# Kernel tuning notes

Measured on AMD Instinct MI355X. Metric: run time of the kernel, lower is better.

Reference implementation:

```python
import jax, jax.numpy as jnp
import numpy as np

N = 100000   # nodes
E = 1000000  # edges
G = 64       # graphs in batch
DIN, DH, DOUT = 128, 128, 64
BN_EPS = 1e-5


def setup_inputs() -> dict:
    key = jax.random.key(0)
    ks = jax.random.split(key, 20)
    inp = {}
    inp['x'] = jax.random.normal(ks[0], (N, DIN), dtype=jnp.float32)
    inp['edge_index'] = jax.random.randint(ks[1], (2, E), 0, N, dtype=jnp.int64)
    inp['batch'] = jnp.sort(jax.random.randint(ks[2], (N,), 0, G, dtype=jnp.int64))
    # GCN conv weights (stored [in, out]) + biases
    s = lambda k, i, o: jax.random.normal(k, (i, o), dtype=jnp.float32) / np.sqrt(i)
    inp['W1'] = s(ks[3], DIN, DH);  inp['b1'] = jnp.zeros((DH,), jnp.float32)
    inp['W2'] = s(ks[4], DH, DH);   inp['b2'] = jnp.zeros((DH,), jnp.float32)
    inp['W3'] = s(ks[5], DH, DOUT); inp['b3'] = jnp.zeros((DOUT,), jnp.float32)
    # BatchNorm params/buffers (eval mode)
    inp['g1'] = jnp.ones((DH,), jnp.float32);  inp['beta1'] = jnp.zeros((DH,), jnp.float32)
    inp['g2'] = jnp.ones((DH,), jnp.float32);  inp['beta2'] = jnp.zeros((DH,), jnp.float32)
    inp['mean1'] = jnp.zeros((DH,), jnp.float32); inp['var1'] = jnp.ones((DH,), jnp.float32)
    inp['mean2'] = jnp.zeros((DH,), jnp.float32); inp['var2'] = jnp.ones((DH,), jnp.float32)
    # GlobalAttention gate_nn: Linear(DOUT,DH) ReLU Linear(DH,1)
    inp['Wg1'] = s(ks[6], DOUT, DH); inp['bg1'] = jnp.zeros((DH,), jnp.float32)
    inp['Wg2'] = s(ks[7], DH, 1);    inp['bg2'] = jnp.zeros((1,), jnp.float32)
    # head MLP: Linear(DOUT,DH) ReLU Linear(DH,DOUT)
    inp['Wm1'] = s(ks[8], DOUT, DH); inp['bm1'] = jnp.zeros((DH,), jnp.float32)
    inp['Wm2'] = s(ks[9], DH, DOUT); inp['bm2'] = jnp.zeros((DOUT,), jnp.float32)
    return inp


def _gcn_conv(x, W, b, src, dst):
    # PyG GCNConv: add self-loops, sym-normalize, linear, scatter-sum, bias
    h = x @ W                                            # [N, out]
    deg = jnp.ones((N,), h.dtype).at[dst].add(1.0)       # in-degree + self-loop
    dinv = jax.lax.rsqrt(deg)
    norm = dinv[src] * dinv[dst]                         # [E]
    msg = h[src] * norm[:, None]                         # gather + scale
    out = jax.ops.segment_sum(msg, dst, num_segments=N)  # scatter
    out = out + h * (dinv * dinv)[:, None]               # self-loop term
    return out + b


def _bn(x, g, beta, mean, var):
    return (x - mean) * jax.lax.rsqrt(var + BN_EPS) * g + beta


def reference(x, edge_index, batch, W1, b1, W2, b2, W3, b3,
              g1, beta1, g2, beta2, mean1, var1, mean2, var2,
              Wg1, bg1, Wg2, bg2, Wm1, bm1, Wm2, bm2):
    src, dst = edge_index[0], edge_index[1]
    h = jax.nn.relu(_bn(_gcn_conv(x, W1, b1, src, dst), g1, beta1, mean1, var1))
    h = jax.nn.relu(_bn(_gcn_conv(h, W2, b2, src, dst), g2, beta2, mean2, var2))
    h = _gcn_conv(h, W3, b3, src, dst)                   # [N, DOUT]
    # GlobalAttention pooling: per-graph softmax of gate scores
    gate = jax.nn.relu(h @ Wg1 + bg1) @ Wg2 + bg2        # [N, 1]
    gate = gate[:, 0]
    m = jax.ops.segment_max(gate, batch, num_segments=G)
    e = jnp.exp(gate - m[batch])
    s = jax.ops.segment_sum(e, batch, num_segments=G)
    a = e / s[batch]                                     # [N]
    pooled = jax.ops.segment_sum(h * a[:, None], batch, num_segments=G)  # [G, DOUT]
    # MLP head (dropout off in eval)
    return jax.nn.relu(pooled @ Wm1 + bm1) @ Wm2 + bm2   # [G, DOUT]
```

## Files before the change

kernel.cpp:

```cpp
#include <hip/hip_runtime.h>
#include <hip/hip_bf16.h>
#include <hip/hip_fp16.h>
#include <math.h>

#define NN 100000
#define EE 1000000
#define GG 64
#define BN_EPS 1e-5f
#define CPB 16
#define EB 4096
#define NBLK ((EE + EB - 1) / EB)
#define NBUCK ((NN + 511) / 512)

typedef __attribute__((ext_vector_type(8))) short bf16x8;
typedef __attribute__((ext_vector_type(4))) float f32x4;

__device__ inline short f2bf(float f) {
  unsigned u = __float_as_uint(f);
  u = u + 0x7fff + ((u >> 16) & 1);
  return (short)(u >> 16);
}
__device__ inline float bf2f(short h) {
  return __uint_as_float(((unsigned)(unsigned short)h) << 16);
}

__device__ inline unsigned fenc(float f) {
  int b = __float_as_int(f);
  return (b < 0) ? ~(unsigned)b : ((unsigned)b | 0x80000000u);
}
__device__ inline float fdec(unsigned u) {
  int b = (u & 0x80000000u) ? (int)(u & 0x7fffffffu) : (int)~u;
  return __int_as_float(b);
}

__device__ inline void acc2(float& a0, float& a1, unsigned u) {
  asm("v_fma_mix_f32 %0, %2, 1.0, %0 op_sel:[0,0,0] op_sel_hi:[1,0,0]\n\t"
      "v_fma_mix_f32 %1, %2, 1.0, %1 op_sel:[1,0,0] op_sel_hi:[1,0,0]"
      : "+v"(a0), "+v"(a1)
      : "v"(u));
}
__device__ inline void acc8(float* a, uint4 u) {
  acc2(a[0], a[1], u.x);
  acc2(a[2], a[3], u.y);
  acc2(a[4], a[5], u.z);
  acc2(a[6], a[7], u.w);
}
__device__ inline uint4 zsel(uint4 u, int ok) {
  uint4 r;
  r.x = ok ? u.x : 0u;
  r.y = ok ? u.y : 0u;
  r.z = ok ? u.z : 0u;
  r.w = ok ? u.w : 0u;
  return r;
}

__global__ __launch_bounds__(256) void k_bhist(const int* __restrict__ dst,
                                               int* __restrict__ bhist, int E) {
  __shared__ int h[256];
  int t = threadIdx.x;
  h[t] = 0;
  __syncthreads();
  int base = blockIdx.x * EB;
#pragma unroll
  for (int j = 0; j < EB / 256; ++j) {
    int i = base + j * 256 + t;
    if (i < E) atomicAdd(&h[dst[i] >> 9], 1);
  }
  __syncthreads();
  bhist[blockIdx.x * 256 + t] = h[t];
}

__global__ __launch_bounds__(256) void k_bscan1(int* __restrict__ bhist,
                                                int* __restrict__ btot) {
  __shared__ int s[256];
  int bin = blockIdx.x, t = threadIdx.x;
  int v = (t < NBLK) ? bhist[t * 256 + bin] : 0;
  s[t] = v;
  __syncthreads();
  for (int o = 1; o < 256; o <<= 1) {
    int u = (t >= o) ? s[t - o] : 0;
    __syncthreads();
    s[t] += u;
    __syncthreads();
  }
  if (t < NBLK) bhist[t * 256 + bin] = s[t] - v;
  if (t == 255) btot[bin] = s[255];
}

__global__ __launch_bounds__(256) void k_bscan2(const int* __restrict__ btot,
                                                int* __restrict__ bstart) {
  __shared__ int s[256];
  int t = threadIdx.x;
  int v = btot[t];
  s[t] = v;
  __syncthreads();
  for (int o = 1; o < 256; o <<= 1) {
    int u = (t >= o) ? s[t - o] : 0;
    __syncthreads();
    s[t] += u;
    __syncthreads();
  }
  bstart[t] = s[t] - v;
}

__global__ __launch_bounds__(256) void k_bscat(const int* __restrict__ src,
                                               const int* __restrict__ dst,
                                               const int* __restrict__ bhist,
                                               const int* __restrict__ bstart,
                                               int2* __restrict__ pairs, int E) {
  __shared__ int h[256];
  __shared__ int base[256];
  int t = threadIdx.x;
  h[t] = 0;
  __syncthreads();
  int b0 = blockIdx.x * EB;
  int ds[EB / 256], rk[EB / 256];
#pragma unroll
  for (int j = 0; j < EB / 256; ++j) {
    int i = b0 + j * 256 + t;
    if (i < E) {
      int d = dst[i];
      ds[j] = d;
      rk[j] = atomicAdd(&h[d >> 9], 1);
    } else
      ds[j] = -1;
  }
  __syncthreads();
  base[t] = bstart[t] + bhist[blockIdx.x * 256 + t];
  __syncthreads();
#pragma unroll
  for (int j = 0; j < EB / 256; ++j) {
    int i = b0 + j * 256 + t;
    if (ds[j] >= 0) {
      int pos = base[ds[j] >> 9] + rk[j];
      pairs[pos] = make_int2(src[i], ds[j]);
    }
  }
}

__global__ __launch_bounds__(256) void k_bfill(const int2* __restrict__ pairs,
                                               const int* __restrict__ bstart,
                                               int* __restrict__ rowstart,
                                               int* __restrict__ eidx,
                                               float* __restrict__ dinv, int N,
                                               int E) {
  __shared__ int h[512];
  __shared__ int ex[512];
  __shared__ int ps[256];
  const int b = blockIdx.x;
  const int n0 = b << 9;
  const int e0 = bstart[b], e1 = bstart[b + 1];
  const int t = threadIdx.x;
  h[t] = 0;
  h[t + 256] = 0;
  __syncthreads();
  for (int i = e0 + t; i < e1; i += 256) atomicAdd(&h[pairs[i].y - n0], 1);
  __syncthreads();
  int v0 = h[2 * t], v1 = h[2 * t + 1];
  int sp = v0 + v1;
  ps[t] = sp;
  __syncthreads();
  for (int o = 1; o < 256; o <<= 1) {
    int u = (t >= o) ? ps[t - o] : 0;
    __syncthreads();
    ps[t] += u;
    __syncthreads();
  }
  int ex0 = ps[t] - sp;
  ex[2 * t] = ex0;
  ex[2 * t + 1] = ex0 + v0;
  __syncthreads();
  for (int i = t; i < 512; i += 256) {
    int node = n0 + i;
    if (node < N) {
      rowstart[node] = e0 + ex[i];
      dinv[node] = rsqrtf(1.0f + (float)h[i]);
    }
  }
  if (b == 0 && t == 0) rowstart[N] = E;
  __syncthreads();
  for (int i = e0 + t; i < e1; i += 256) {
    int2 p = pairs[i];
    int r = atomicAdd(&ex[p.y - n0], 1);
    eidx[e0 + r] = p.x;
  }
}

__global__ __launch_bounds__(256) void k_prep(
    const float* __restrict__ W1, const float* __restrict__ W2,
    const float* __restrict__ W3, const float* __restrict__ Wg1,
    short* __restrict__ wt, const float* __restrict__ g1,
    const float* __restrict__ b1, const float* __restrict__ m1,
    const float* __restrict__ v1, const float* __restrict__ g2,
    const float* __restrict__ b2, const float* __restrict__ m2,
    const float* __restrict__ v2, float* __restrict__ s1,
    float* __restrict__ h1, float* __restrict__ s2, float* __restrict__ h2,
    const int* __restrict__ batch, int* __restrict__ gstart,
    float* __restrict__ pooledw, int N) {
  const int b = blockIdx.x, t = threadIdx.x;
  if (b < 192) {
    int i = b * 256 + t;
    const float* W;
    short *hi, *lo;
    int K, M, idx;
    if (i < 16384) {
      W = W1; hi = wt; lo = wt + 16384; K = 128; M = 128; idx = i;
    } else if (i < 32768) {
      W = W2; hi = wt + 32768; lo = wt + 49152; K = 128; M = 128; idx = i - 16384;
    } else if (i < 40960) {
      W = W3; hi = wt + 65536; lo = wt + 73728; K = 128; M = 64; idx = i - 32768;
    } else {
      W = Wg1; hi = wt + 81920; lo = wt + 90112; K = 64; M = 128; idx = i - 40960;
    }
    int k = idx / M, n = idx % M;
    float w = W[idx];
    short h = f2bf(w);
    hi[n * K + k] = h;
    lo[n * K + k] = f2bf(w - bf2f(h));
  } else if (b == 192) {
    if (t < 128) {
      float s = g1[t] * rsqrtf(v1[t] + BN_EPS);
      s1[t] = s;
      h1[t] = b1[t] - m1[t] * s;
    } else {
      int j = t - 128;
      float s = g2[j] * rsqrtf(v2[j] + BN_EPS);
      s2[j] = s;
      h2[j] = b2[j] - m2[j] * s;
    }
  } else {
    if (t <= GG) {
      int lo = 0, hi = N;
      while (lo < hi) {
        int mid = (lo + hi) >> 1;
        if (batch[mid] < t) lo = mid + 1;
        else hi = mid;
      }
      gstart[t] = lo;
    }
    for (int i = t; i < GG * 64 + GG + GG; i += 256) pooledw[i] = 0.f;
  }
}

template <int K, int M, int CTB, int AIN, int DINV, int GATE, int OUTH>
__device__ __forceinline__ void mgemm_body(
    short* lds, const float* __restrict__ Xf, const short* __restrict__ Xhi,
    const short* __restrict__ Xlo, const short* __restrict__ Wthi,
    const short* __restrict__ Wtlo, const float* __restrict__ dinv,
    const float* __restrict__ gbias, const float* __restrict__ Wg2v,
    const float* __restrict__ bg2v, void* __restrict__ Y,
    float* __restrict__ gate, int nrows) {
  constexpr int NC = K / 32;
  constexpr int KP = K + 8;
  constexpr int R = 2;
  const int lane = threadIdx.x & 63;
  const int wave = threadIdx.x >> 6;
  const int m16 = lane & 15;
  const int quad = lane >> 4;
  const int rowbase = blockIdx.x * 128 + wave * 32;
  const int cbase = blockIdx.y * CTB * 16;

  bf16x8 ahi[R][NC], alo[R][NC];
#pragma unroll
  for (int t = 0; t < R; ++t) {
    const int arow = rowbase + t * 16 + m16;
    const bool rok = arow < nrows;
#pragma unroll
    for (int c = 0; c < NC; ++c) {
      const int k0 = c * 32 + quad * 8;
      if constexpr (AIN) {
        if (rok) {
          ahi[t][c] = *(const bf16x8*)(Xhi + (size_t)arow * K + k0);
          alo[t][c] = *(const bf16x8*)(Xlo + (size_t)arow * K + k0);
        } else {
          ahi[t][c] = bf16x8{0, 0, 0, 0, 0, 0, 0, 0};
          alo[t][c] = bf16x8{0, 0, 0, 0, 0, 0, 0, 0};
        }
      } else {
        float4 v0 = make_float4(0.f, 0.f, 0.f, 0.f), v1 = v0;
        if (rok) {
          v0 = *(const float4*)(Xf + (size_t)arow * K + k0);
          v1 = *(const float4*)(Xf + (size_t)arow * K + k0 + 4);
        }
        float vv[8] = {v0.x, v0.y, v0.z, v0.w, v1.x, v1.y, v1.z, v1.w};
#pragma unroll
        for (int j = 0; j < 8; ++j) {
          short h = f2bf(vv[j]);
          ahi[t][c][j] = h;
          alo[t][c][j] = f2bf(vv[j] - bf2f(h));
        }
      }
    }
  }

  {
    constexpr int ELEMS = CTB * 16 * K;
#pragma unroll
    for (int i = threadIdx.x * 8; i < ELEMS; i += 256 * 8) {
      const int r = i / K, c = i % K;
      *(bf16x8*)(&lds[r * KP + c]) =
          *(const bf16x8*)(Wthi + (size_t)(cbase + r) * K + c);
      *(bf16x8*)(&lds[CTB * 16 * KP + r * KP + c]) =
          *(const bf16x8*)(Wtlo + (size_t)(cbase + r) * K + c);
    }
  }

  float dv[R][4];
  if constexpr (DINV && !GATE) {
#pragma unroll
    for (int t = 0; t < R; ++t)
#pragma unroll
      for (int r = 0; r < 4; ++r) {
        int row = rowbase + t * 16 + quad * 4 + r;
        dv[t][r] = (row < nrows) ? dinv[row] : 0.f;
      }
  }

  float gp[R][4];
  if constexpr (GATE) {
#pragma unroll
    for (int t = 0; t < R; ++t)
#pragma unroll
      for (int r = 0; r < 4; ++r) gp[t][r] = 0.f;
  }

  __syncthreads();

  f32x4 accs[CTB][R];
#pragma unroll
  for (int ct = 0; ct < CTB; ++ct) {
    bf16x8 bhi[NC], blo[NC];
    const int wrow = (ct * 16 + m16) * KP + quad * 8;
#pragma unroll
    for (int c = 0; c < NC; ++c) {
      bhi[c] = *(const bf16x8*)(&lds[wrow + c * 32]);
      blo[c] = *(const bf16x8*)(&lds[CTB * 16 * KP + wrow + c * 32]);
    }
#pragma unroll
    for (int t = 0; t < R; ++t) {
      f32x4 acc = {0.f, 0.f, 0.f, 0.f};
#pragma unroll
      for (int c = 0; c < NC; ++c) {
        acc = __builtin_amdgcn_mfma_f32_16x16x32_bf16(ahi[t][c], bhi[c], acc, 0, 0, 0);
        acc = __builtin_amdgcn_mfma_f32_16x16x32_bf16(ahi[t][c], blo[c], acc, 0, 0, 0);
        acc = __builtin_amdgcn_mfma_f32_16x16x32_bf16(alo[t][c], bhi[c], acc, 0, 0, 0);
      }
      if constexpr (GATE) {
        const int col = cbase + ct * 16 + m16;
        const float gb = gbias[col], wg = Wg2v[col];
#pragma unroll
        for (int r = 0; r < 4; ++r) gp[t][r] += fmaxf(acc[r] + gb, 0.f) * wg;
      } else {
        accs[ct][t] = acc;
      }
    }
  }

  if constexpr (GATE) {
#pragma unroll
    for (int o = 1; o < 16; o <<= 1) {
#pragma unroll
      for (int t = 0; t < R; ++t)
#pragma unroll
        for (int r = 0; r < 4; ++r) gp[t][r] += __shfl_xor(gp[t][r], o, 64);
    }
    if (m16 == 0) {
      const float b2 = bg2v[0];
#pragma unroll
      for (int t = 0; t < R; ++t)
#pragma unroll
        for (int r = 0; r < 4; ++r) {
          const int row = rowbase + t * 16 + quad * 4 + r;
          if (row < nrows) gate[row] = gp[t][r] + b2;
        }
    }
  } else {
    constexpr int COLS = CTB * 16;
    constexpr int SP = COLS + 8;
    __syncthreads();
#pragma unroll
    for (int ct = 0; ct < CTB; ++ct)
#pragma unroll
      for (int t = 0; t < R; ++t)
#pragma unroll
        for (int r = 0; r < 4; ++r) {
          const int row_l = wave * 32 + t * 16 + quad * 4 + r;
          float v = accs[ct][t][r];
          if constexpr (DINV) v *= dv[t][r];
          __half hv = __float2half(v);
          lds[row_l * SP + ct * 16 + m16] = *(short*)&hv;
        }
    __syncthreads();
    constexpr int TOT = 128 * COLS;
#pragma unroll
    for (int p = 0; p < TOT / (256 * 8); ++p) {
      const int idx8 = (p * 256 + threadIdx.x) * 8;
      const int row_l = idx8 / COLS;
      const int col0 = idx8 % COLS;
      const int grow = blockIdx.x * 128 + row_l;
      if (grow < nrows) {
        bf16x8 v = *(const bf16x8*)(&lds[row_l * SP + col0]);
        *(bf16x8*)((__half*)Y + (size_t)grow * M + cbase + col0) = v;
      }
    }
  }
}

#define MGEMM_ARGS                                                            \
  const float *Xf, const short *Xhi, const short *Xlo, const short *Wthi,     \
      const short *Wtlo, const float *dinv, const float *gbias,               \
      const float *Wg2v, const float *bg2v, void *Y, float *gate, int nrows

#define DEF_MGEMM(NAME, K, M, CTB, AIN, DINV, GATE, OUTH, WPE)                \
  __global__ __launch_bounds__(256, WPE) void NAME(MGEMM_ARGS) {              \
    __shared__ short lds[2 * CTB * 16 * (K + 8)];                             \
    mgemm_body<K, M, CTB, AIN, DINV, GATE, OUTH>(lds, Xf, Xhi, Xlo, Wthi,     \
                                                 Wtlo, dinv, gbias, Wg2v,     \
                                                 bg2v, Y, gate, nrows);       \
  }

DEF_MGEMM(k_mgemm1, 128, 128, 2, 0, 1, 0, 1, 4)
DEF_MGEMM(k_mgemm2, 128, 128, 2, 1, 1, 0, 1, 4)
DEF_MGEMM(k_mgemm3, 128, 64, 2, 1, 1, 0, 1, 4)
DEF_MGEMM(k_mgemmg, 64, 128, 8, 0, 0, 1, 0, 3)

template <int M, int EPI>
__device__ __forceinline__ void agg_body(
    const __half* __restrict__ hp, const int* __restrict__ rowstart,
    const int* __restrict__ eidx, const float* __restrict__ dinv,
    const float* __restrict__ bias, const float* __restrict__ bns,
    const float* __restrict__ bnh, float* __restrict__ outf,
    short* __restrict__ ohi, short* __restrict__ olo, int N) {
  constexpr int LPR = M / 8;
  constexpr int NPW = 64 / (2 * LPR);
  const int wv = (blockIdx.x * 256 + threadIdx.x) >> 6;
  const int lane = threadIdx.x & 63;
  const int grp = lane / (2 * LPR);
  const int slot = (lane / LPR) & 1;
  const int sub = lane % LPR;
  const int w = wv * NPW + grp;
  if (w >= N) return;
  const unsigned subo = (unsigned)sub * 16u;
  const float di = dinv[w];
  const int lo = rowstart[w], hi = rowstart[w + 1];
  const int hi1 = hi - 1;
  const char* hpb = (const char*)hp;
  float a[8] = {0.f, 0.f, 0.f, 0.f, 0.f, 0.f, 0.f, 0.f};

  int e = lo + slot;
  while (e < hi) {
    int idx[8], ss[8];
    uint4 uu[8];
#pragma unroll
    for (int p = 0; p < 8; ++p) {
      idx[p] = e + 2 * p;
      ss[p] = eidx[min(idx[p], hi1)];
    }
#pragma unroll
    for (int p = 0; p < 8; ++p)
      uu[p] = *(const uint4*)(hpb + ((unsigned)ss[p] * (unsigned)(M * 2) + subo));
#pragma unroll
    for (int p = 0; p < 8; ++p) {
      uu[p] = zsel(uu[p], idx[p] < hi);
      acc8(a, uu[p]);
    }
    e += 16;
  }
#pragma unroll
  for (int j = 0; j < 8; ++j) a[j] += __shfl_xor(a[j], LPR, 64);

  if (slot != 0) return;
  uint4 us = *(const uint4*)(hpb + ((unsigned)w * (unsigned)(M * 2) + subo));
  acc8(a, us);
  float4 b0 = *(const float4*)(bias + sub * 8);
  float4 b1 = *(const float4*)(bias + sub * 8 + 4);
  float r[8];
  r[0] = a[0] * di + b0.x;
  r[1] = a[1] * di + b0.y;
  r[2] = a[2] * di + b0.z;
  r[3] = a[3] * di + b0.w;
  r[4] = a[4] * di + b1.x;
  r[5] = a[5] * di + b1.y;
  r[6] = a[6] * di + b1.z;
  r[7] = a[7] * di + b1.w;
  if constexpr (EPI) {
    float4 s0 = *(const float4*)(bns + sub * 8);
    float4 s1 = *(const float4*)(bns + sub * 8 + 4);
    float4 h0 = *(const float4*)(bnh + sub * 8);
    float4 h1 = *(const float4*)(bnh + sub * 8 + 4);
    float sv[8] = {s0.x, s0.y, s0.z, s0.w, s1.x, s1.y, s1.z, s1.w};
    float hv[8] = {h0.x, h0.y, h0.z, h0.w, h1.x, h1.y, h1.z, h1.w};
    short hs[8], ls[8];
#pragma unroll
    for (int j = 0; j < 8; ++j) {
      float ev = fmaxf(r[j] * sv[j] + hv[j], 0.f);
      short hb = f2bf(ev);
      float res = ev - bf2f(hb);
      hs[j] = hb;
      ls[j] = (short)(__float_as_uint(res) >> 16);
    }
    *(short4*)(ohi + (size_t)w * M + sub * 8) = make_short4(hs[0], hs[1], hs[2], hs[3]);
    *(short4*)(ohi + (size_t)w * M + sub * 8 + 4) = make_short4(hs[4], hs[5], hs[6], hs[7]);
    *(short4*)(olo + (size_t)w * M + sub * 8) = make_short4(ls[0], ls[1], ls[2], ls[3]);
    *(short4*)(olo + (size_t)w * M + sub * 8 + 4) = make_short4(ls[4], ls[5], ls[6], ls[7]);
  } else {
    *(float4*)(outf + (size_t)w * M + sub * 8) = make_float4(r[0], r[1], r[2], r[3]);
    *(float4*)(outf + (size_t)w * M + sub * 8 + 4) = make_float4(r[4], r[5], r[6], r[7]);
  }
}

#define AGG_ARGS                                                              \
  const __half *hp, const int *rowstart, const int *eidx, const float *dinv,  \
      const float *bias, const float *bns, const float *bnh, float *outf,     \
      short *ohi, short *olo, int N

#define DEF_AGG(NAME, M, EPI)                                                 \
  __global__ __launch_bounds__(256) void NAME(AGG_ARGS) {                     \
    agg_body<M, EPI>(hp, rowstart, eidx, dinv, bias, bns, bnh, outf, ohi,     \
                     olo, N);                                                 \
  }

DEF_AGG(k_agg1, 128, 1)
DEF_AGG(k_agg2, 128, 1)
DEF_AGG(k_agg3, 64, 0)

__global__ __launch_bounds__(256) void k_pmax(const float* __restrict__ gate,
                                              const int* __restrict__ gstart,
                                              unsigned* __restrict__ gmaxu) {
  __shared__ unsigned red[256];
  const int g = blockIdx.x / CPB;
  const int c = blockIdx.x % CPB;
  const int lo = gstart[g], hi = gstart[g + 1];
  const int len = hi - lo;
  const int b0 = lo + (int)(((long long)len * c) / CPB);
  const int b1 = lo + (int)(((long long)len * (c + 1)) / CPB);
  unsigned mx = 0u;
  for (int i = b0 + threadIdx.x; i < b1; i += 256) mx = max(mx, fenc(gate[i]));
  red[threadIdx.x] = mx;
  __syncthreads();
  for (int o = 128; o; o >>= 1) {
    if (threadIdx.x < o)
      red[threadIdx.x] = max(red[threadIdx.x], red[threadIdx.x + o]);
    __syncthreads();
  }
  if (threadIdx.x == 0 && red[0] != 0u) atomicMax(&gmaxu[g], red[0]);
}

__global__ __launch_bounds__(256) void k_psum(const float* __restrict__ gate,
                                              const float* __restrict__ h3,
                                              const unsigned* __restrict__ gmaxu,
                                              const int* __restrict__ gstart,
                                              float* __restrict__ pooledw,
                                              float* __restrict__ ssum) {
  __shared__ float accs[4][64];
  __shared__ float ses[4];
  const int g = blockIdx.x / CPB;
  const int c = blockIdx.x % CPB;
  const int lo = gstart[g], hi = gstart[g + 1];
  const int len = hi - lo;
  const int b0 = lo + (int)(((long long)len * c) / CPB);
  const int b1 = lo + (int)(((long long)len * (c + 1)) / CPB);
  const int wave = threadIdx.x >> 6, lane = threadIdx.x & 63;
  const float m = fdec(gmaxu[g]);
  float acc = 0.f, se = 0.f;
  for (int i = b0 + wave; i < b1; i += 4) {
    float e = expf(gate[i] - m);
    acc += e * h3[(size_t)i * 64 + lane];
    se += e;
  }
  accs[wave][lane] = acc;
  if (lane == 0) ses[wave] = se;
  __syncthreads();
  if (threadIdx.x < 64) {
    float a = accs[0][threadIdx.x] + accs[1][threadIdx.x] +
              accs[2][threadIdx.x] + accs[3][threadIdx.x];
    if (a != 0.f) atomicAdd(&pooledw[g * 64 + threadIdx.x], a);
  }
  if (threadIdx.x == 64) {
    float s = ses[0] + ses[1] + ses[2] + ses[3];
    if (s != 0.f) atomicAdd(&ssum[g], s);
  }
}

__global__ __launch_bounds__(256) void k_head(const float* __restrict__ pooledw,
                                              const float* __restrict__ ssum,
                                              const float* __restrict__ Wm1,
                                              const float* __restrict__ bm1,
                                              const float* __restrict__ Wm2,
                                              const float* __restrict__ bm2,
                                              float* __restrict__ out) {
  __shared__ float P[64 * 64];
  __shared__ float T[64 * 128];
  int tid = threadIdx.x;
  for (int i = tid; i < 4096; i += 256) {
    float s = ssum[i >> 6];
    P[i] = pooledw[i] * ((s > 0.f) ? 1.0f / s : 0.f);
  }
  __syncthreads();
  for (int e = tid; e < 8192; e += 256) {
    int r = e >> 7, c = e & 127;
    float a = bm1[c];
    for (int k = 0; k < 64; ++k) a += P[r * 64 + k] * Wm1[k * 128 + c];
    T[e] = fmaxf(a, 0.f);
  }
  __syncthreads();
  for (int e = tid; e < 4096; e += 256) {
    int r = e >> 6, c = e & 63;
    float a = bm2[c];
    for (int k = 0; k < 128; ++k) a += T[r * 128 + k] * Wm2[k * 64 + c];
    out[e] = a;
  }
}

extern "C" void kernel_launch(void* const* d_in, const int* in_sizes, int n_in,
                              void* d_out, int out_size, void* d_ws,
                              size_t ws_size, hipStream_t stream) {
  const int N = NN, E = EE;
  const float* x = (const float*)d_in[0];
  const int* ei = (const int*)d_in[1];
  const int* batch = (const int*)d_in[2];
  const float* W1 = (const float*)d_in[3];
  const float* b1 = (const float*)d_in[4];
  const float* W2 = (const float*)d_in[5];
  const float* b2 = (const float*)d_in[6];
  const float* W3 = (const float*)d_in[7];
  const float* b3 = (const float*)d_in[8];
  const float* g1 = (const float*)d_in[9];
  const float* beta1 = (const float*)d_in[10];
  const float* g2 = (const float*)d_in[11];
  const float* beta2 = (const float*)d_in[12];
  const float* mean1 = (const float*)d_in[13];
  const float* var1 = (const float*)d_in[14];
  const float* mean2 = (const float*)d_in[15];
  const float* var2 = (const float*)d_in[16];
  const float* Wg1 = (const float*)d_in[17];
  const float* bg1 = (const float*)d_in[18];
  const float* Wg2 = (const float*)d_in[19];
  const float* bg2 = (const float*)d_in[20];
  const float* Wm1 = (const float*)d_in[21];
  const float* bm1 = (const float*)d_in[22];
  const float* Wm2 = (const float*)d_in[23];
  const float* bm2 = (const float*)d_in[24];
  float* out = (float*)d_out;

  const int* src = ei;
  const int* dst = ei + E;

  char* wsb = (char*)d_ws;
  size_t off = 0;
  auto alloc = [&](size_t elems) -> void* {
    void* p = wsb + off;
    off += elems * 4;
    return p;
  };
  int* rowstart = (int*)alloc(N + 4);
  int* eidx = (int*)alloc(E);
  int2* pairs = (int2*)alloc((size_t)E * 2);
  int* bhist = (int*)alloc(NBLK * 256 + 256);
  int* btot = (int*)alloc(256);
  int* bstart = (int*)alloc(256);
  float* dinv = (float*)alloc(N);
  float* gate = (float*)alloc(N);
  __half* hbuf = (__half*)alloc((size_t)N * 64);
  short* ahi_p = (short*)alloc((size_t)N * 64);
  short* alo_p = (short*)alloc((size_t)N * 64);
  float* fbuf = (float*)alloc((size_t)N * 64);
  short* wt = (short*)alloc(49152);
  float* bn1s = (float*)alloc(128);
  float* bn1h = (float*)alloc(128);
  float* bn2s = (float*)alloc(128);
  float* bn2h = (float*)alloc(128);
  float* pooledw = (float*)alloc(GG * 64);
  float* ssum = (float*)alloc(GG);
  unsigned* gmaxu = (unsigned*)alloc(GG);
  int* gstart = (int*)alloc(GG + 4);
  (void)ws_size;
  (void)n_in;
  (void)in_sizes;
  (void)out_size;

  k_bhist<<<NBLK, 256, 0, stream>>>(dst, bhist, E);
  k_bscan1<<<256, 256, 0, stream>>>(bhist, btot);
  k_bscan2<<<1, 256, 0, stream>>>(btot, bstart);
  k_bscat<<<NBLK, 256, 0, stream>>>(src, dst, bhist, bstart, pairs, E);
  k_bfill<<<NBUCK, 256, 0, stream>>>(pairs, bstart, rowstart, eidx, dinv, N, E);

  k_prep<<<194, 256, 0, stream>>>(W1, W2, W3, Wg1, wt, g1, beta1, mean1, var1,
                                  g2, beta2, mean2, var2, bn1s, bn1h, bn2s,
                                  bn2h, batch, gstart, pooledw, N);

  const int gbb = (N + 127) / 128;
  const int ab128 = (N + 7) / 8;
  const int ab64 = (N + 15) / 16;

  k_mgemm1<<<dim3(gbb, 4), 256, 0, stream>>>(
      x, nullptr, nullptr, wt, wt + 16384, dinv, nullptr, nullptr, nullptr,
      hbuf, nullptr, N);
  k_agg1<<<ab128, 256, 0, stream>>>(hbuf, rowstart, eidx, dinv, b1, bn1s,
                                    bn1h, nullptr, ahi_p, alo_p, N);

  k_mgemm2<<<dim3(gbb, 4), 256, 0, stream>>>(
      nullptr, ahi_p, alo_p, wt + 32768, wt + 49152, dinv, nullptr, nullptr,
      nullptr, hbuf, nullptr, N);
  k_agg2<<<ab128, 256, 0, stream>>>(hbuf, rowstart, eidx, dinv, b2, bn2s,
                                    bn2h, nullptr, ahi_p, alo_p, N);

  k_mgemm3<<<dim3(gbb, 2), 256, 0, stream>>>(
      nullptr, ahi_p, alo_p, wt + 65536, wt + 73728, dinv, nullptr, nullptr,
      nullptr, hbuf, nullptr, N);
  k_agg3<<<ab64, 256, 0, stream>>>(hbuf, rowstart, eidx, dinv, b3, nullptr,
                                   nullptr, fbuf, nullptr, nullptr, N);

  k_mgemmg<<<dim3(gbb, 1), 256, 0, stream>>>(
      fbuf, nullptr, nullptr, wt + 81920, wt + 90112, nullptr, bg1, Wg2, bg2,
      nullptr, gate, N);

  k_pmax<<<GG * CPB, 256, 0, stream>>>(gate, gstart, gmaxu);
  k_psum<<<GG * CPB, 256, 0, stream>>>(gate, fbuf, gmaxu, gstart, pooledw,
                                       ssum);

  k_head<<<1, 256, 0, stream>>>(pooledw, ssum, Wm1, bm1, Wm2, bm2, out);
}
```

Before: 509.8 us.

## Fuse gate MLP into layer-3 aggregation and widen GEMM column tiles

Removes the separate gate GEMM kernel by computing the gate score (Linear-ReLU-Linear) inside the third aggregation kernel. Each block aggregates 16 nodes into LDS as split bf16 hi/lo values, then one wave runs MFMAs against Wg1 read from global memory. This saves one launch and a full re-read of the layer-3 features. The GEMMs also double CTB from 2 to 4 so each block covers more output columns, halving the grid's y-dimension, and launch bounds drop to 3 waves per EU. The fused tail leaves three of four waves idle during the gate MFMA, and the larger tiles raise LDS and register use.

```diff
diff --git a/kernel.cpp b/kernel.cpp
--- a/kernel.cpp
+++ b/kernel.cpp
@@ -242,14 +242,12 @@
   }
 }
 
-template <int K, int M, int CTB, int AIN, int DINV, int GATE, int OUTH>
+template <int K, int M, int CTB, int AIN, int DINV, int OUTH>
 __device__ __forceinline__ void mgemm_body(
     short* lds, const float* __restrict__ Xf, const short* __restrict__ Xhi,
     const short* __restrict__ Xlo, const short* __restrict__ Wthi,
     const short* __restrict__ Wtlo, const float* __restrict__ dinv,
-    const float* __restrict__ gbias, const float* __restrict__ Wg2v,
-    const float* __restrict__ bg2v, void* __restrict__ Y,
-    float* __restrict__ gate, int nrows) {
+    void* __restrict__ Y, int nrows) {
   constexpr int NC = K / 32;
   constexpr int KP = K + 8;
   constexpr int R = 2;
@@ -306,7 +304,7 @@
   }
 
   float dv[R][4];
-  if constexpr (DINV && !GATE) {
+  if constexpr (DINV) {
 #pragma unroll
     for (int t = 0; t < R; ++t)
 #pragma unroll
@@ -314,14 +312,6 @@
         int row = rowbase + t * 16 + quad * 4 + r;
         dv[t][r] = (row < nrows) ? dinv[row] : 0.f;
       }
-  }
-
-  float gp[R][4];
-  if constexpr (GATE) {
-#pragma unroll
-    for (int t = 0; t < R; ++t)
-#pragma unroll
-      for (int r = 0; r < 4; ++r) gp[t][r] = 0.f;
   }
 
   __syncthreads();
@@ -345,84 +335,54 @@
         acc = __builtin_amdgcn_mfma_f32_16x16x32_bf16(ahi[t][c], blo[c], acc, 0, 0, 0);
         acc = __builtin_amdgcn_mfma_f32_16x16x32_bf16(alo[t][c], bhi[c], acc, 0, 0, 0);
       }
-      if constexpr (GATE) {
-        const int col = cbase + ct * 16 + m16;
-        const float gb = gbias[col], wg = Wg2v[col];
-#pragma unroll
-        for (int r = 0; r < 4; ++r) gp[t][r] += fmaxf(acc[r] + gb, 0.f) * wg;
-      } else {
-        accs[ct][t] = acc;
+      accs[ct][t] = acc;
+    }
+  }
+
+  constexpr int COLS = CTB * 16;
+  constexpr int SP = COLS + 8;
+  __syncthreads();
+#pragma unroll
+  for (int ct = 0; ct < CTB; ++ct)
+#pragma unroll
+    for (int t = 0; t < R; ++t)
+#pragma unroll
+      for (int r = 0; r < 4; ++r) {
+        const int row_l = wave * 32 + t * 16 + quad * 4 + r;
+        float v = accs[ct][t][r];
+        if constexpr (DINV) v *= dv[t][r];
+        __half hv = __float2half(v);
+        lds[row_l * SP + ct * 16 + m16] = *(short*)&hv;
       }
-    }
-  }
-
-  if constexpr (GATE) {
-#pragma unroll
-    for (int o = 1; o < 16; o <<= 1) {
-#pragma unroll
-      for (int t = 0; t < R; ++t)
-#pragma unroll
-        for (int r = 0; r < 4; ++r) gp[t][r] += __shfl_xor(gp[t][r], o, 64);
-    }
-    if (m16 == 0) {
-      const float b2 = bg2v[0];
-#pragma unroll
-      for (int t = 0; t < R; ++t)
-#pragma unroll
-        for (int r = 0; r < 4; ++r) {
-          const int row = rowbase + t * 16 + quad * 4 + r;
-          if (row < nrows) gate[row] = gp[t][r] + b2;
-        }
-    }
-  } else {
-    constexpr int COLS = CTB * 16;
-    constexpr int SP = COLS + 8;
-    __syncthreads();
-#pragma unroll
-    for (int ct = 0; ct < CTB; ++ct)
-#pragma unroll
-      for (int t = 0; t < R; ++t)
-#pragma unroll
-        for (int r = 0; r < 4; ++r) {
-          const int row_l = wave * 32 + t * 16 + quad * 4 + r;
-          float v = accs[ct][t][r];
-          if constexpr (DINV) v *= dv[t][r];
-          __half hv = __float2half(v);
-          lds[row_l * SP + ct * 16 + m16] = *(short*)&hv;
-        }
-    __syncthreads();
-    constexpr int TOT = 128 * COLS;
-#pragma unroll
-    for (int p = 0; p < TOT / (256 * 8); ++p) {
-      const int idx8 = (p * 256 + threadIdx.x) * 8;
-      const int row_l = idx8 / COLS;
-      const int col0 = idx8 % COLS;
-      const int grow = blockIdx.x * 128 + row_l;
-      if (grow < nrows) {
-        bf16x8 v = *(const bf16x8*)(&lds[row_l * SP + col0]);
-        *(bf16x8*)((__half*)Y + (size_t)grow * M + cbase + col0) = v;
-      }
+  __syncthreads();
+  constexpr int TOT = 128 * COLS;
+#pragma unroll
+  for (int p = 0; p < TOT / (256 * 8); ++p) {
+    const int idx8 = (p * 256 + threadIdx.x) * 8;
+    const int row_l = idx8 / COLS;
+    const int col0 = idx8 % COLS;
+    const int grow = blockIdx.x * 128 + row_l;
+    if (grow < nrows) {
+      bf16x8 v = *(const bf16x8*)(&lds[row_l * SP + col0]);
+      *(bf16x8*)((__half*)Y + (size_t)grow * M + cbase + col0) = v;
     }
   }
 }
 
 #define MGEMM_ARGS                                                            \
   const float *Xf, const short *Xhi, const short *Xlo, const short *Wthi,     \
-      const short *Wtlo, const float *dinv, const float *gbias,               \
-      const float *Wg2v, const float *bg2v, void *Y, float *gate, int nrows
-
-#define DEF_MGEMM(NAME, K, M, CTB, AIN, DINV, GATE, OUTH, WPE)                \
-  __global__ __launch_bounds__(256, WPE) void NAME(MGEMM_ARGS) {              \
+      const short *Wtlo, const float *dinv, void *Y, int nrows
+
+#define DEF_MGEMM(NAME, K, M, CTB, AIN, DINV, OUTH)                           \
+  __global__ __launch_bounds__(256, 3) void NAME(MGEMM_ARGS) {                \
     __shared__ short lds[2 * CTB * 16 * (K + 8)];                             \
-    mgemm_body<K, M, CTB, AIN, DINV, GATE, OUTH>(lds, Xf, Xhi, Xlo, Wthi,     \
-                                                 Wtlo, dinv, gbias, Wg2v,     \
-                                                 bg2v, Y, gate, nrows);       \
-  }
-
-DEF_MGEMM(k_mgemm1, 128, 128, 2, 0, 1, 0, 1, 4)
-DEF_MGEMM(k_mgemm2, 128, 128, 2, 1, 1, 0, 1, 4)
-DEF_MGEMM(k_mgemm3, 128, 64, 2, 1, 1, 0, 1, 4)
-DEF_MGEMM(k_mgemmg, 64, 128, 8, 0, 0, 1, 0, 3)
+    mgemm_body<K, M, CTB, AIN, DINV, OUTH>(lds, Xf, Xhi, Xlo, Wthi, Wtlo,     \
+                                           dinv, Y, nrows);                   \
+  }
+
+DEF_MGEMM(k_mgemm1, 128, 128, 4, 0, 1, 1)
+DEF_MGEMM(k_mgemm2, 128, 128, 4, 1, 1, 1)
+DEF_MGEMM(k_mgemm3, 128, 64, 4, 1, 1, 1)
 
 template <int M, int EPI>
 __device__ __forceinline__ void agg_body(
@@ -522,7 +482,132 @@
 
 DEF_AGG(k_agg1, 128, 1)
 DEF_AGG(k_agg2, 128, 1)
-DEF_AGG(k_agg3, 64, 0)
+
+__global__ __launch_bounds__(256) void k_agg3g(
+    const __half* __restrict__ hp, const int* __restrict__ rowstart,
+    const int* __restrict__ eidx, const float* __restrict__ dinv,
+    const float* __restrict__ bias, const short* __restrict__ wg1hi,
+    const short* __restrict__ wg1lo, const float* __restrict__ bg1,
+    const float* __restrict__ Wg2v, const float* __restrict__ bg2v,
+    float* __restrict__ outf, float* __restrict__ gate, int N) {
+  __shared__ short Ahi[16][72];
+  __shared__ short Alo[16][72];
+  const int lane = threadIdx.x & 63;
+  const int wv = threadIdx.x >> 6;
+  const int grp = lane >> 4;
+  const int slot = (lane >> 3) & 1;
+  const int sub = lane & 7;
+  const int node_l = wv * 4 + grp;
+  const int w = blockIdx.x * 16 + node_l;
+  const bool valid = w < N;
+
+  for (int i = threadIdx.x; i < 16 * 72; i += 256) {
+    (&Ahi[0][0])[i] = 0;
+    (&Alo[0][0])[i] = 0;
+  }
+  __syncthreads();
+
+  const unsigned subo = (unsigned)sub * 16u;
+  const float di = valid ? dinv[w] : 0.f;
+  const int lo = valid ? rowstart[w] : 0;
+  const int hi = valid ? rowstart[w + 1] : 0;
+  const int hi1 = hi - 1;
+  const char* hpb = (const char*)hp;
+  float a[8] = {0.f, 0.f, 0.f, 0.f, 0.f, 0.f, 0.f, 0.f};
+
+  int e = lo + slot;
+  while (e < hi) {
+    int idx[8], ss[8];
+    uint4 uu[8];
+#pragma unroll
+    for (int p = 0; p < 8; ++p) {
+      idx[p] = e + 2 * p;
+      ss[p] = eidx[min(idx[p], hi1)];
+    }
+#pragma unroll
+    for (int p = 0; p < 8; ++p)
+      uu[p] = *(const uint4*)(hpb + ((unsigned)ss[p] * 128u + subo));
+#pragma unroll
+    for (int p = 0; p < 8; ++p) {
+      uu[p] = zsel(uu[p], idx[p] < hi);
+      acc8(a, uu[p]);
+    }
+    e += 16;
+  }
+#pragma unroll
+  for (int j = 0; j < 8; ++j) a[j] += __shfl_xor(a[j], 8, 64);
+
+  if (slot == 0 && valid) {
+    uint4 us = *(const uint4*)(hpb + ((unsigned)w * 128u + subo));
+    acc8(a, us);
+    float4 b0 = *(const float4*)(bias + sub * 8);
+    float4 b1 = *(const float4*)(bias + sub * 8 + 4);
+    float r[8];
+    r[0] = a[0] * di + b0.x;
+    r[1] = a[1] * di + b0.y;
+    r[2] = a[2] * di + b0.z;
+    r[3] = a[3] * di + b0.w;
+    r[4] = a[4] * di + b1.x;
+    r[5] = a[5] * di + b1.y;
+    r[6] = a[6] * di + b1.z;
+    r[7] = a[7] * di + b1.w;
+    *(float4*)(outf + (size_t)w * 64 + sub * 8) =
+        make_float4(r[0], r[1], r[2], r[3]);
+    *(float4*)(outf + (size_t)w * 64 + sub * 8 + 4) =
+        make_float4(r[4], r[5], r[6], r[7]);
+#pragma unroll
+    for (int j = 0; j < 8; ++j) {
+      short h = f2bf(r[j]);
+      Ahi[node_l][sub * 8 + j] = h;
+      Alo[node_l][sub * 8 + j] = f2bf(r[j] - bf2f(h));
+    }
+  }
+  __syncthreads();
+
+  if (wv != 0) return;
+  const int m16 = lane & 15;
+  const int quad = lane >> 4;
+  bf16x8 fa_hi[2], fa_lo[2];
+#pragma unroll
+  for (int c = 0; c < 2; ++c) {
+    fa_hi[c] = *(const bf16x8*)(&Ahi[m16][c * 32 + quad * 8]);
+    fa_lo[c] = *(const bf16x8*)(&Alo[m16][c * 32 + quad * 8]);
+  }
+  float gp[4] = {0.f, 0.f, 0.f, 0.f};
+#pragma unroll
+  for (int ct = 0; ct < 8; ++ct) {
+    bf16x8 bhi[2], blo[2];
+    const int wrow = (ct * 16 + m16) * 64 + quad * 8;
+#pragma unroll
+    for (int c = 0; c < 2; ++c) {
+      bhi[c] = *(const bf16x8*)(wg1hi + wrow + c * 32);
+      blo[c] = *(const bf16x8*)(wg1lo + wrow + c * 32);
+    }
+    f32x4 acc = {0.f, 0.f, 0.f, 0.f};
+#pragma unroll
+    for (int c = 0; c < 2; ++c) {
+      acc = __builtin_amdgcn_mfma_f32_16x16x32_bf16(fa_hi[c], bhi[c], acc, 0, 0, 0);
+      acc = __builtin_amdgcn_mfma_f32_16x16x32_bf16(fa_hi[c], blo[c], acc, 0, 0, 0);
+      acc = __builtin_amdgcn_mfma_f32_16x16x32_bf16(fa_lo[c], bhi[c], acc, 0, 0, 0);
+    }
+    const int col = ct * 16 + m16;
+    const float gb = bg1[col], wg = Wg2v[col];
+#pragma unroll
+    for (int r = 0; r < 4; ++r) gp[r] += fmaxf(acc[r] + gb, 0.f) * wg;
+  }
+#pragma unroll
+  for (int o = 1; o < 16; o <<= 1)
+#pragma unroll
+    for (int r = 0; r < 4; ++r) gp[r] += __shfl_xor(gp[r], o, 64);
+  if (m16 == 0) {
+    const float b2 = bg2v[0];
+#pragma unroll
+    for (int r = 0; r < 4; ++r) {
+      const int node = blockIdx.x * 16 + quad * 4 + r;
+      if (node < N) gate[node] = gp[r] + b2;
+    }
+  }
+}
 
 __global__ __launch_bounds__(256) void k_pmax(const float* __restrict__ gate,
                                               const int* __restrict__ gstart,
@@ -691,29 +776,23 @@
 
   const int gbb = (N + 127) / 128;
   const int ab128 = (N + 7) / 8;
-  const int ab64 = (N + 15) / 16;
-
-  k_mgemm1<<<dim3(gbb, 4), 256, 0, stream>>>(
-      x, nullptr, nullptr, wt, wt + 16384, dinv, nullptr, nullptr, nullptr,
-      hbuf, nullptr, N);
+  const int ab16 = (N + 15) / 16;
+
+  k_mgemm1<<<dim3(gbb, 2), 256, 0, stream>>>(x, nullptr, nullptr, wt,
+                                             wt + 16384, dinv, hbuf, N);
   k_agg1<<<ab128, 256, 0, stream>>>(hbuf, rowstart, eidx, dinv, b1, bn1s,
                                     bn1h, nullptr, ahi_p, alo_p, N);
 
-  k_mgemm2<<<dim3(gbb, 4), 256, 0, stream>>>(
-      nullptr, ahi_p, alo_p, wt + 32768, wt + 49152, dinv, nullptr, nullptr,
-      nullptr, hbuf, nullptr, N);
+  k_mgemm2<<<dim3(gbb, 2), 256, 0, stream>>>(nullptr, ahi_p, alo_p, wt + 32768,
+                                             wt + 49152, dinv, hbuf, N);
   k_agg2<<<ab128, 256, 0, stream>>>(hbuf, rowstart, eidx, dinv, b2, bn2s,
                                     bn2h, nullptr, ahi_p, alo_p, N);
 
-  k_mgemm3<<<dim3(gbb, 2), 256, 0, stream>>>(
-      nullptr, ahi_p, alo_p, wt + 65536, wt + 73728, dinv, nullptr, nullptr,
-      nullptr, hbuf, nullptr, N);
-  k_agg3<<<ab64, 256, 0, stream>>>(hbuf, rowstart, eidx, dinv, b3, nullptr,
-                                   nullptr, fbuf, nullptr, nullptr, N);
-
-  k_mgemmg<<<dim3(gbb, 1), 256, 0, stream>>>(
-      fbuf, nullptr, nullptr, wt + 81920, wt + 90112, nullptr, bg1, Wg2, bg2,
-      nullptr, gate, N);
+  k_mgemm3<<<dim3(gbb, 1), 256, 0, stream>>>(nullptr, ahi_p, alo_p, wt + 65536,
+                                             wt + 73728, dinv, hbuf, N);
+  k_agg3g<<<ab16, 256, 0, stream>>>(hbuf, rowstart, eidx, dinv, b3,
+                                    wt + 81920, wt + 90112, bg1, Wg2, bg2,
+                                    fbuf, gate, N);
 
   k_pmax<<<GG * CPB, 256, 0, stream>>>(gate, gstart, gmaxu);
   k_psum<<<GG * CPB, 256, 0, stream>>>(gate, fbuf, gmaxu, gstart, pooledw,
```

New measurement: 455.6 us. 1.12x faster.
